# Kernel optimization log

Hardware: AMD Instinct MI355X
Metric: run time of the kernel (lower is better)

The kernel has to match this reference:

```python
import jax, jax.numpy as jnp
import numpy as np

# ---- module hyperparams (match init_kwargs) ----
IN_CH, OUT_CH = 32, 64
KERNEL = 9
STRIDE, PADDING = 1, 4
GRID_SIZE, SPLINE_ORDER = 5, 3
GRID_LO, GRID_HI = -1.0, 1.0
NUM_COEF = GRID_SIZE + SPLINE_ORDER  # 8 spline basis functions


def make_grid():
    h = (GRID_HI - GRID_LO) / GRID_SIZE
    # extended knot vector, same for every input feature (efficient-KAN)
    return (jnp.arange(-SPLINE_ORDER, GRID_SIZE + SPLINE_ORDER + 1, dtype=jnp.float32) * h + GRID_LO)


def b_splines(x, grid, order):
    """Cox-de Boor B-spline bases. x: (...,) -> (..., NUM_COEF)."""
    x = x[..., None]
    bases = ((x >= grid[:-1]) & (x < grid[1:])).astype(x.dtype)
    for k in range(1, order + 1):
        left = (x - grid[: -(k + 1)]) / (grid[k:-1] - grid[: -(k + 1)])
        right = (grid[k + 1:] - x) / (grid[k + 1:] - grid[1:-k])
        bases = left * bases[..., :-1] + right * bases[..., 1:]
    return bases


def setup_inputs() -> dict:
    key = jax.random.key(0)
    k1, k2, k3, k4 = jax.random.split(key, 4)
    x = jax.random.normal(k1, (16, IN_CH, 2048), dtype=jnp.float32)
    # all O*I KANLinear(kernel->1) modules batched into single tensors
    base_w = jax.random.normal(k2, (OUT_CH, IN_CH, KERNEL), dtype=jnp.float32) * (1.0 / np.sqrt(KERNEL))
    spline_w = jax.random.normal(k3, (OUT_CH, IN_CH, KERNEL, NUM_COEF), dtype=jnp.float32) * 0.1
    spline_scaler = jax.random.normal(k4, (OUT_CH, IN_CH, KERNEL), dtype=jnp.float32) * (1.0 / np.sqrt(KERNEL))
    return {"x": x, "base_w": base_w, "spline_w": spline_w, "spline_scaler": spline_scaler}


def reference(x, base_w, spline_w, spline_scaler):
    grid = make_grid()
    B, I, L = x.shape
    L_out = (L + 2 * PADDING - (KERNEL - 1) - 1) // STRIDE + 1  # dilation=1
    xp = jnp.pad(x, ((0, 0), (0, 0), (PADDING, PADDING)))
    # sliding windows: (B, I, L_out, K)
    idx = jnp.arange(L_out)[:, None] * STRIDE + jnp.arange(KERNEL)[None, :]
    win = xp[:, :, idx]
    # base branch: silu(window) . base_weight, summed over in_channels
    out = jnp.einsum('bilk,oik->bol', jax.nn.silu(win), base_w)
    # spline branch
    bs = b_splines(win, grid, SPLINE_ORDER)          # (B, I, L_out, K, C)
    sw = spline_w * spline_scaler[..., None]         # scaled spline weight
    out = out + jnp.einsum('bilkc,oikc->bol', bs, sw)
    return out
```

## Files before the change

### kernel.cpp

```cpp
#include <hip/hip_runtime.h>
#include <hip/hip_bf16.h>

namespace {

constexpr int KIN  = 32;
constexpr int KOUT = 64;
constexpr int KW   = 9;
constexpr int KPAD = 4;
constexpr int LIN  = 2048;
constexpr int KTOT = 2592;

typedef __bf16 bf16x8 __attribute__((ext_vector_type(8)));
typedef float  f32x4  __attribute__((ext_vector_type(4)));
typedef unsigned short u16x4 __attribute__((ext_vector_type(4)));
typedef unsigned short u16x8 __attribute__((ext_vector_type(8)));

__device__ __forceinline__ unsigned short f2bf(float x) {
    unsigned int u = __float_as_uint(x);
    u += 0x7FFFu + ((u >> 16) & 1u);
    return (unsigned short)(u >> 16);
}

__device__ __forceinline__ float bf2f(unsigned short h) {
    return __uint_as_float((unsigned int)h << 16);
}

#define MFMA16(a, b, c) __builtin_amdgcn_mfma_f32_16x16x32_bf16((a), (b), (c), 0, 0, 0)

__global__ __launch_bounds__(256) void kan_wprep(const float* __restrict__ base_w,
                                                 const float* __restrict__ spline_w,
                                                 const float* __restrict__ spline_scaler,
                                                 unsigned short* __restrict__ Wf) {
    unsigned int idx = blockIdx.x * 256 + threadIdx.x;
    unsigned int ch  = idx >> 8;
    unsigned int m   = (idx >> 6) & 3;
    unsigned int lane = idx & 63;
    unsigned int hi = lane >> 4, lo = lane & 15;
    unsigned int o  = m * 16 + lo;
    unsigned int kb = ch * 32 + hi * 8;

    u16x8 pk;
#pragma unroll
    for (int e = 0; e < 8; ++e) {
        unsigned int kappa = kb + e;
        unsigned int k  = kappa / 288;
        unsigned int r2 = kappa - k * 288;
        unsigned int i  = r2 / 9;
        unsigned int c  = r2 - i * 9;
        unsigned int t  = o * 288 + i * 9 + k;
        float val = (c == 0) ? base_w[t]
                             : spline_w[(size_t)t * 8 + (c - 1)] * spline_scaler[t];
        pk[e] = f2bf(val);
    }
    *(u16x8*)(Wf + (size_t)idx * 8) = pk;
}

constexpr int BN     = 64;
constexpr int TROW   = 72;
constexpr int F2COLS = 296;

__global__ __launch_bounds__(512, 4) void kan_fused(const float* __restrict__ x,
                                                    const unsigned short* __restrict__ Wf,
                                                    float* __restrict__ out) {
    __shared__ __align__(16) char smem[TROW * F2COLS * 2];
    unsigned short* f2t = (unsigned short*)smem;

    int tid  = threadIdx.x;
    int lane = tid & 63;
    int wv   = tid >> 6;
    int lo = lane & 15, hi = lane >> 4;

    int blk = blockIdx.x;
    int b   = blk >> 5;
    int l0  = (blk & 31) * BN;

    float vv[5];
#pragma unroll
    for (int p = 0; p < 5; ++p) {
        int unit = p * 512 + tid;
        bool ok = unit < TROW * KIN;
        int i = unit / TROW;
        int r = unit - i * TROW;
        int gx = l0 + r - KPAD;
        vv[p] = 0.f;
        if (ok && gx >= 0 && gx < LIN) vv[p] = x[((size_t)b * KIN + i) * LIN + gx];
    }

    {
        f32x4 z = (f32x4){0.f, 0.f, 0.f, 0.f};
        for (int c = tid; c < TROW * F2COLS / 8; c += 512)
            *(f32x4*)(f2t + (size_t)c * 8) = z;
    }
    __syncthreads();

#pragma unroll
    for (int p = 0; p < 5; ++p) {
        int unit = p * 512 + tid;
        bool ok = unit < TROW * KIN;
        int i = unit / TROW;
        int r = unit - i * TROW;
        float v = vv[p];
        if (ok) {
            unsigned short* row = f2t + (size_t)r * F2COLS + i * 9;
            row[0] = f2bf(v / (1.f + __expf(-v)));
            float t5 = (v + 2.2f) * 2.5f;
            float mf = floorf(t5);
            int   m  = (int)mf;
            float u  = t5 - mf;
            float u2 = u * u, u3 = u2 * u;
            float w  = 1.f - u;
            float P0 = u3 * (1.f / 6.f);
            float P3 = w * w * w * (1.f / 6.f);
            float P1 = (1.f / 6.f) + 0.5f * u + 0.5f * u2 - 0.5f * u3;
            float P2 = (4.f / 6.f) - u2 + 0.5f * u3;
            int c0 = m - 3;
            if ((unsigned)(c0 + 0) <= 7u) row[1 + c0 + 0] = f2bf(P3);
            if ((unsigned)(c0 + 1) <= 7u) row[1 + c0 + 1] = f2bf(P2);
            if ((unsigned)(c0 + 2) <= 7u) row[1 + c0 + 2] = f2bf(P1);
            if ((unsigned)(c0 + 3) <= 7u) row[1 + c0 + 3] = f2bf(P0);
        }
    }
    __syncthreads();

    const int ch0 = 10 * wv;
    constexpr int NCHW = 10;

    f32x4 acc[4][4];
#pragma unroll
    for (int m = 0; m < 4; ++m)
#pragma unroll
        for (int n = 0; n < 4; ++n) acc[m][n] = (f32x4){0.f, 0.f, 0.f, 0.f};

    int kk = ch0 / 9;
    int jb = ch0 - kk * 9;
    const unsigned short* wp = Wf + (size_t)ch0 * 2048 + (size_t)lane * 8;
    const unsigned short* fp = f2t + (size_t)(lo + kk) * F2COLS + jb * 32 + hi * 8;

    bf16x8 a0 = *(const bf16x8*)(wp);
    bf16x8 a1 = *(const bf16x8*)(wp + 512);
    bf16x8 a2 = *(const bf16x8*)(wp + 1024);
    bf16x8 a3 = *(const bf16x8*)(wp + 1536);
    bf16x8 b0 = *(const bf16x8*)(fp);
    bf16x8 b1 = *(const bf16x8*)(fp + 16 * F2COLS);
    bf16x8 b2 = *(const bf16x8*)(fp + 32 * F2COLS);
    bf16x8 b3 = *(const bf16x8*)(fp + 48 * F2COLS);

    for (int t = 0; t < NCHW; ++t) {
        bool last = (t + 1 == NCHW);
        const unsigned short* wpn = last ? wp : wp + 2048;
        int jb2 = last ? jb : jb + 1;
        const unsigned short* fpn = last ? fp : fp + ((jb2 == 9) ? (F2COLS - 8 * 32) : 32);
        if (jb2 == 9) jb2 = 0;

        bf16x8 na0 = *(const bf16x8*)(wpn);
        bf16x8 na1 = *(const bf16x8*)(wpn + 512);
        bf16x8 na2 = *(const bf16x8*)(wpn + 1024);
        bf16x8 na3 = *(const bf16x8*)(wpn + 1536);

        __builtin_amdgcn_s_setprio(1);
        acc[0][0] = MFMA16(a0, b0, acc[0][0]);
        acc[1][0] = MFMA16(a1, b0, acc[1][0]);
        acc[2][0] = MFMA16(a2, b0, acc[2][0]);
        acc[3][0] = MFMA16(a3, b0, acc[3][0]);
        b0 = *(const bf16x8*)(fpn);
        acc[0][1] = MFMA16(a0, b1, acc[0][1]);
        acc[1][1] = MFMA16(a1, b1, acc[1][1]);
        acc[2][1] = MFMA16(a2, b1, acc[2][1]);
        acc[3][1] = MFMA16(a3, b1, acc[3][1]);
        b1 = *(const bf16x8*)(fpn + 16 * F2COLS);
        acc[0][2] = MFMA16(a0, b2, acc[0][2]);
        acc[1][2] = MFMA16(a1, b2, acc[1][2]);
        acc[2][2] = MFMA16(a2, b2, acc[2][2]);
        acc[3][2] = MFMA16(a3, b2, acc[3][2]);
        b2 = *(const bf16x8*)(fpn + 32 * F2COLS);
        acc[0][3] = MFMA16(a0, b3, acc[0][3]);
        acc[1][3] = MFMA16(a1, b3, acc[1][3]);
        acc[2][3] = MFMA16(a2, b3, acc[2][3]);
        acc[3][3] = MFMA16(a3, b3, acc[3][3]);
        b3 = *(const bf16x8*)(fpn + 48 * F2COLS);
        __builtin_amdgcn_s_setprio(0);

        a0 = na0; a1 = na1; a2 = na2; a3 = na3;
        wp = wpn; fp = fpn; jb = jb2;
    }

    {
        int mq = wv & 3;
        int np = wv >> 2;
        bf16x8 a80 = *(const bf16x8*)(Wf + (size_t)80 * 2048 + (size_t)mq * 512 + (size_t)lane * 8);
        const unsigned short* fp80 = f2t + (size_t)(lo + 8) * F2COLS + 8 * 32 + hi * 8;
        bf16x8 bA = *(const bf16x8*)(fp80 + (size_t)(2 * np) * 16 * F2COLS);
        bf16x8 bB = *(const bf16x8*)(fp80 + (size_t)(2 * np + 1) * 16 * F2COLS);
        switch (wv) {
        case 0: acc[0][0] = MFMA16(a80, bA, acc[0][0]); acc[0][1] = MFMA16(a80, bB, acc[0][1]); break;
        case 1: acc[1][0] = MFMA16(a80, bA, acc[1][0]); acc[1][1] = MFMA16(a80, bB, acc[1][1]); break;
        case 2: acc[2][0] = MFMA16(a80, bA, acc[2][0]); acc[2][1] = MFMA16(a80, bB, acc[2][1]); break;
        case 3: acc[3][0] = MFMA16(a80, bA, acc[3][0]); acc[3][1] = MFMA16(a80, bB, acc[3][1]); break;
        case 4: acc[0][2] = MFMA16(a80, bA, acc[0][2]); acc[0][3] = MFMA16(a80, bB, acc[0][3]); break;
        case 5: acc[1][2] = MFMA16(a80, bA, acc[1][2]); acc[1][3] = MFMA16(a80, bB, acc[1][3]); break;
        case 6: acc[2][2] = MFMA16(a80, bA, acc[2][2]); acc[2][3] = MFMA16(a80, bB, acc[2][3]); break;
        case 7: acc[3][2] = MFMA16(a80, bA, acc[3][2]); acc[3][3] = MFMA16(a80, bB, acc[3][3]); break;
        }
    }

    __syncthreads();
    unsigned short* red16 = (unsigned short*)smem;
#pragma unroll
    for (int mp = 0; mp < 2; ++mp) {
#pragma unroll
        for (int dm = 0; dm < 2; ++dm)
#pragma unroll
            for (int n = 0; n < 4; ++n) {
                f32x4 a = acc[mp * 2 + dm][n];
                u16x4 pk = (u16x4){f2bf(a[0]), f2bf(a[1]), f2bf(a[2]), f2bf(a[3])};
                *(u16x4*)(red16 + (((size_t)wv * 8 + dm * 4 + n) * 64 + lane) * 4) = pk;
            }
        __syncthreads();
        {
            int dm = wv >> 2, n = wv & 3;
            f32x4 s = (f32x4){0.f, 0.f, 0.f, 0.f};
#pragma unroll
            for (int w = 0; w < 8; ++w) {
                u16x4 pk = *(const u16x4*)(red16 + (((size_t)w * 8 + dm * 4 + n) * 64 + lane) * 4);
                s[0] += bf2f(pk[0]);
                s[1] += bf2f(pk[1]);
                s[2] += bf2f(pk[2]);
                s[3] += bf2f(pk[3]);
            }
            int o = (mp * 2 + dm) * 16 + hi * 4;
            float* op = out + ((size_t)b * KOUT + o) * LIN + l0 + n * 16 + lo;
            op[0]               = s[0];
            op[LIN]             = s[1];
            op[2 * LIN]         = s[2];
            op[3 * (size_t)LIN] = s[3];
        }
        if (mp == 0) __syncthreads();
    }
}

}

extern "C" void kernel_launch(void* const* d_in, const int* in_sizes, int n_in,
                              void* d_out, int out_size, void* d_ws, size_t ws_size,
                              hipStream_t stream) {
    const float* x             = (const float*)d_in[0];
    const float* base_w        = (const float*)d_in[1];
    const float* spline_w      = (const float*)d_in[2];
    const float* spline_scaler = (const float*)d_in[3];
    float* out = (float*)d_out;

    unsigned short* Wf = (unsigned short*)d_ws;

    kan_wprep<<<81, 256, 0, stream>>>(base_w, spline_w, spline_scaler, Wf);
    kan_fused<<<512, 512, 0, stream>>>(x, Wf, out);
}
```

Before: 23.15 us.

## Fuse weight prep into main kernel with cross-block sentinel spin-wait

Removes the separate weight-prep launch: the first 81 blocks of the main kernel build the bf16 fused weight matrix and publish a per-block sentinel flag. All blocks build their B-spline tile first, then spin on the flags before the MFMA loop. This targets the launch gap and the serialization between the two kernels. The flags are never reset, so on later calls blocks may not wait for the current rewrite. The acquire side uses only relaxed loads, so memory ordering is weak.

```diff
diff --git a/kernel.cpp b/kernel.cpp
--- a/kernel.cpp
+++ b/kernel.cpp
@@ -9,6 +9,7 @@
 constexpr int KPAD = 4;
 constexpr int LIN  = 2048;
 constexpr int KTOT = 2592;
+constexpr unsigned MAGIC = 0x7F7F7F7Fu;
 
 typedef __bf16 bf16x8 __attribute__((ext_vector_type(8)));
 typedef float  f32x4  __attribute__((ext_vector_type(4)));
@@ -27,41 +28,17 @@
 
 #define MFMA16(a, b, c) __builtin_amdgcn_mfma_f32_16x16x32_bf16((a), (b), (c), 0, 0, 0)
 
-__global__ __launch_bounds__(256) void kan_wprep(const float* __restrict__ base_w,
-                                                 const float* __restrict__ spline_w,
-                                                 const float* __restrict__ spline_scaler,
-                                                 unsigned short* __restrict__ Wf) {
-    unsigned int idx = blockIdx.x * 256 + threadIdx.x;
-    unsigned int ch  = idx >> 8;
-    unsigned int m   = (idx >> 6) & 3;
-    unsigned int lane = idx & 63;
-    unsigned int hi = lane >> 4, lo = lane & 15;
-    unsigned int o  = m * 16 + lo;
-    unsigned int kb = ch * 32 + hi * 8;
-
-    u16x8 pk;
-#pragma unroll
-    for (int e = 0; e < 8; ++e) {
-        unsigned int kappa = kb + e;
-        unsigned int k  = kappa / 288;
-        unsigned int r2 = kappa - k * 288;
-        unsigned int i  = r2 / 9;
-        unsigned int c  = r2 - i * 9;
-        unsigned int t  = o * 288 + i * 9 + k;
-        float val = (c == 0) ? base_w[t]
-                             : spline_w[(size_t)t * 8 + (c - 1)] * spline_scaler[t];
-        pk[e] = f2bf(val);
-    }
-    *(u16x8*)(Wf + (size_t)idx * 8) = pk;
-}
-
 constexpr int BN     = 64;
 constexpr int TROW   = 72;
 constexpr int F2COLS = 296;
 
-__global__ __launch_bounds__(512, 4) void kan_fused(const float* __restrict__ x,
-                                                    const unsigned short* __restrict__ Wf,
-                                                    float* __restrict__ out) {
+__global__ __launch_bounds__(512, 4) void kan_all(const float* __restrict__ x,
+                                                  const float* __restrict__ base_w,
+                                                  const float* __restrict__ spline_w,
+                                                  const float* __restrict__ spline_scaler,
+                                                  unsigned short* __restrict__ Wf,
+                                                  unsigned int* __restrict__ sent,
+                                                  float* __restrict__ out) {
     __shared__ __align__(16) char smem[TROW * F2COLS * 2];
     unsigned short* f2t = (unsigned short*)smem;
 
@@ -73,6 +50,34 @@
     int blk = blockIdx.x;
     int b   = blk >> 5;
     int l0  = (blk & 31) * BN;
+
+    if (blk < 81) {
+        if (tid < 256) {
+            unsigned idx  = (unsigned)blk * 256 + tid;
+            unsigned m    = (idx >> 6) & 3;
+            unsigned ln   = idx & 63;
+            unsigned o    = m * 16 + (ln & 15);
+            unsigned kb   = (unsigned)blk * 32 + (ln >> 4) * 8;
+            u16x8 pk;
+#pragma unroll
+            for (int e = 0; e < 8; ++e) {
+                unsigned kappa = kb + e;
+                unsigned k  = kappa / 288;
+                unsigned r2 = kappa - k * 288;
+                unsigned i  = r2 / 9;
+                unsigned c  = r2 - i * 9;
+                unsigned t  = o * 288 + i * 9 + k;
+                float val = (c == 0) ? base_w[t]
+                                     : spline_w[(size_t)t * 8 + (c - 1)] * spline_scaler[t];
+                pk[e] = f2bf(val);
+            }
+            *(u16x8*)(Wf + (size_t)idx * 8) = pk;
+        }
+        __builtin_amdgcn_fence(__ATOMIC_RELEASE, "agent");
+        __syncthreads();
+        if (tid == 0)
+            __hip_atomic_store(&sent[blk], MAGIC, __ATOMIC_RELAXED, __HIP_MEMORY_SCOPE_AGENT);
+    }
 
     float vv[5];
 #pragma unroll
@@ -122,6 +127,13 @@
     }
     __syncthreads();
 
+    if (tid < 81) {
+        while (__hip_atomic_load(&sent[tid], __ATOMIC_RELAXED, __HIP_MEMORY_SCOPE_AGENT) != MAGIC)
+            __builtin_amdgcn_s_sleep(2);
+    }
+    __syncthreads();
+    asm volatile("" ::: "memory");
+
     const int ch0 = 10 * wv;
     constexpr int NCHW = 10;
 
@@ -249,8 +261,8 @@
     const float* spline_scaler = (const float*)d_in[3];
     float* out = (float*)d_out;
 
-    unsigned short* Wf = (unsigned short*)d_ws;
-
-    kan_wprep<<<81, 256, 0, stream>>>(base_w, spline_w, spline_scaler, Wf);
-    kan_fused<<<512, 512, 0, stream>>>(x, Wf, out);
-}
+    unsigned short* Wf  = (unsigned short*)d_ws;
+    unsigned int*  sent = (unsigned int*)((char*)d_ws + 331776);
+
+    kan_all<<<512, 512, 0, stream>>>(x, base_w, spline_w, spline_scaler, Wf, sent, out);
+}
```

New measurement: 32.52 us. 1.41x slower.

## Double output tile to 128 columns with 1024-thread blocks and hoisted weight loads

Applied to the files above, without the earlier changes.

Each block now covers 128 output positions with 16 waves: pairs of waves share a K-chunk and split the N dimension into two 64-column halves. This halves the grid to 256 blocks and amortizes the feature-tile halo over more columns. The initial weight-fragment loads are moved ahead of the feature construction so their global latency overlaps the LDS fill. The cross-wave reduction is restructured into two phases, one per half. The risk is a larger LDS footprint per block (about 80 KB) and fewer blocks than CUs, which may hurt occupancy and parallelism.

```diff
diff --git a/kernel.cpp b/kernel.cpp
--- a/kernel.cpp
+++ b/kernel.cpp
@@ -35,9 +35,8 @@
     unsigned int ch  = idx >> 8;
     unsigned int m   = (idx >> 6) & 3;
     unsigned int lane = idx & 63;
-    unsigned int hi = lane >> 4, lo = lane & 15;
-    unsigned int o  = m * 16 + lo;
-    unsigned int kb = ch * 32 + hi * 8;
+    unsigned int o  = m * 16 + (lane & 15);
+    unsigned int kb = ch * 32 + (lane >> 4) * 8;
 
     u16x8 pk;
 #pragma unroll
@@ -55,13 +54,13 @@
     *(u16x8*)(Wf + (size_t)idx * 8) = pk;
 }
 
-constexpr int BN     = 64;
-constexpr int TROW   = 72;
+constexpr int BN     = 128;
+constexpr int TROW   = 136;
 constexpr int F2COLS = 296;
 
-__global__ __launch_bounds__(512, 4) void kan_fused(const float* __restrict__ x,
-                                                    const unsigned short* __restrict__ Wf,
-                                                    float* __restrict__ out) {
+__global__ __launch_bounds__(1024, 4) void kan_fused(const float* __restrict__ x,
+                                                     const unsigned short* __restrict__ Wf,
+                                                     float* __restrict__ out) {
     __shared__ __align__(16) char smem[TROW * F2COLS * 2];
     unsigned short* f2t = (unsigned short*)smem;
 
@@ -69,15 +68,27 @@
     int lane = tid & 63;
     int wv   = tid >> 6;
     int lo = lane & 15, hi = lane >> 4;
+    int kg = wv >> 1;
+    int nh = wv & 1;
 
     int blk = blockIdx.x;
-    int b   = blk >> 5;
-    int l0  = (blk & 31) * BN;
+    int b   = blk >> 4;
+    int l0  = (blk & 15) * BN;
+
+    const int ch0 = 10 * kg;
+    constexpr int NCHW = 10;
+    int kk = ch0 / 9;
+    int jb = ch0 - kk * 9;
+    const unsigned short* wp = Wf + (size_t)ch0 * 2048 + (size_t)lane * 8;
+    bf16x8 a0 = *(const bf16x8*)(wp);
+    bf16x8 a1 = *(const bf16x8*)(wp + 512);
+    bf16x8 a2 = *(const bf16x8*)(wp + 1024);
+    bf16x8 a3 = *(const bf16x8*)(wp + 1536);
 
     float vv[5];
 #pragma unroll
     for (int p = 0; p < 5; ++p) {
-        int unit = p * 512 + tid;
+        int unit = p * 1024 + tid;
         bool ok = unit < TROW * KIN;
         int i = unit / TROW;
         int r = unit - i * TROW;
@@ -88,14 +99,14 @@
 
     {
         f32x4 z = (f32x4){0.f, 0.f, 0.f, 0.f};
-        for (int c = tid; c < TROW * F2COLS / 8; c += 512)
+        for (int c = tid; c < TROW * F2COLS / 8; c += 1024)
             *(f32x4*)(f2t + (size_t)c * 8) = z;
     }
     __syncthreads();
 
 #pragma unroll
     for (int p = 0; p < 5; ++p) {
-        int unit = p * 512 + tid;
+        int unit = p * 1024 + tid;
         bool ok = unit < TROW * KIN;
         int i = unit / TROW;
         int r = unit - i * TROW;
@@ -122,24 +133,13 @@
     }
     __syncthreads();
 
-    const int ch0 = 10 * wv;
-    constexpr int NCHW = 10;
-
     f32x4 acc[4][4];
 #pragma unroll
     for (int m = 0; m < 4; ++m)
 #pragma unroll
         for (int n = 0; n < 4; ++n) acc[m][n] = (f32x4){0.f, 0.f, 0.f, 0.f};
 
-    int kk = ch0 / 9;
-    int jb = ch0 - kk * 9;
-    const unsigned short* wp = Wf + (size_t)ch0 * 2048 + (size_t)lane * 8;
-    const unsigned short* fp = f2t + (size_t)(lo + kk) * F2COLS + jb * 32 + hi * 8;
-
-    bf16x8 a0 = *(const bf16x8*)(wp);
-    bf16x8 a1 = *(const bf16x8*)(wp + 512);
-    bf16x8 a2 = *(const bf16x8*)(wp + 1024);
-    bf16x8 a3 = *(const bf16x8*)(wp + 1536);
+    const unsigned short* fp = f2t + (size_t)(nh * 64 + lo + kk) * F2COLS + jb * 32 + hi * 8;
     bf16x8 b0 = *(const bf16x8*)(fp);
     bf16x8 b1 = *(const bf16x8*)(fp + 16 * F2COLS);
     bf16x8 b2 = *(const bf16x8*)(fp + 32 * F2COLS);
@@ -185,13 +185,13 @@
     }
 
     {
-        int mq = wv & 3;
-        int np = wv >> 2;
+        int mq = kg & 3;
+        int np = kg >> 2;
         bf16x8 a80 = *(const bf16x8*)(Wf + (size_t)80 * 2048 + (size_t)mq * 512 + (size_t)lane * 8);
-        const unsigned short* fp80 = f2t + (size_t)(lo + 8) * F2COLS + 8 * 32 + hi * 8;
+        const unsigned short* fp80 = f2t + (size_t)(nh * 64 + lo + 8) * F2COLS + 8 * 32 + hi * 8;
         bf16x8 bA = *(const bf16x8*)(fp80 + (size_t)(2 * np) * 16 * F2COLS);
         bf16x8 bB = *(const bf16x8*)(fp80 + (size_t)(2 * np + 1) * 16 * F2COLS);
-        switch (wv) {
+        switch (kg) {
         case 0: acc[0][0] = MFMA16(a80, bA, acc[0][0]); acc[0][1] = MFMA16(a80, bB, acc[0][1]); break;
         case 1: acc[1][0] = MFMA16(a80, bA, acc[1][0]); acc[1][1] = MFMA16(a80, bB, acc[1][1]); break;
         case 2: acc[2][0] = MFMA16(a80, bA, acc[2][0]); acc[2][1] = MFMA16(a80, bB, acc[2][1]); break;
@@ -206,35 +206,39 @@
     __syncthreads();
     unsigned short* red16 = (unsigned short*)smem;
 #pragma unroll
-    for (int mp = 0; mp < 2; ++mp) {
-#pragma unroll
-        for (int dm = 0; dm < 2; ++dm)
-#pragma unroll
-            for (int n = 0; n < 4; ++n) {
-                f32x4 a = acc[mp * 2 + dm][n];
-                u16x4 pk = (u16x4){f2bf(a[0]), f2bf(a[1]), f2bf(a[2]), f2bf(a[3])};
-                *(u16x4*)(red16 + (((size_t)wv * 8 + dm * 4 + n) * 64 + lane) * 4) = pk;
-            }
+    for (int ph = 0; ph < 2; ++ph) {
+        if (nh == ph) {
+#pragma unroll
+            for (int m = 0; m < 4; ++m)
+#pragma unroll
+                for (int n = 0; n < 4; ++n) {
+                    int sid = m * 4 + n;
+                    f32x4 a = acc[m][n];
+                    u16x4 pk = (u16x4){f2bf(a[0]), f2bf(a[1]), f2bf(a[2]), f2bf(a[3])};
+                    *(u16x4*)(red16 + (((size_t)sid * 8 + kg) * 64 + lane) * 4) = pk;
+                }
+        }
         __syncthreads();
         {
-            int dm = wv >> 2, n = wv & 3;
+            int sid = wv;
+            int m = sid >> 2, n = sid & 3;
             f32x4 s = (f32x4){0.f, 0.f, 0.f, 0.f};
 #pragma unroll
             for (int w = 0; w < 8; ++w) {
-                u16x4 pk = *(const u16x4*)(red16 + (((size_t)w * 8 + dm * 4 + n) * 64 + lane) * 4);
+                u16x4 pk = *(const u16x4*)(red16 + (((size_t)sid * 8 + w) * 64 + lane) * 4);
                 s[0] += bf2f(pk[0]);
                 s[1] += bf2f(pk[1]);
                 s[2] += bf2f(pk[2]);
                 s[3] += bf2f(pk[3]);
             }
-            int o = (mp * 2 + dm) * 16 + hi * 4;
-            float* op = out + ((size_t)b * KOUT + o) * LIN + l0 + n * 16 + lo;
+            int o = m * 16 + hi * 4;
+            float* op = out + ((size_t)b * KOUT + o) * LIN + l0 + ph * 64 + n * 16 + lo;
             op[0]               = s[0];
             op[LIN]             = s[1];
             op[2 * LIN]         = s[2];
             op[3 * (size_t)LIN] = s[3];
         }
-        if (mp == 0) __syncthreads();
+        if (ph == 0) __syncthreads();
     }
 }
 
@@ -252,5 +256,5 @@
     unsigned short* Wf = (unsigned short*)d_ws;
 
     kan_wprep<<<81, 256, 0, stream>>>(base_w, spline_w, spline_scaler, Wf);
-    kan_fused<<<512, 512, 0, stream>>>(x, Wf, out);
-}
+    kan_fused<<<256, 1024, 0, stream>>>(x, Wf, out);
+}
```

Result: slower. 24.67 us (+6.6%).

## Switch GEMM core to 32x32x16 bf16 MFMA tiles

Applied to the files above, without the earlier changes.

Replaces the 16x16x32 MFMA tiling with 32x32x16 bf16 MFMA, so each wave holds four 32x32 accumulators instead of sixteen 16x16 ones. The weight prep layout, the LDS feature indexing, the tail chunk handling and the cross-wave reduction are all rewritten to match the new fragment layout. Weight A-fragment loads are also issued earlier, before the spline-basis construction, to hide global latency. The intent is fewer MFMA issues and fewer operand loads per FLOP. The cost is longer per-instruction latency over a short 20-step loop, plus new reduction indexing.

```diff
diff --git a/kernel.cpp b/kernel.cpp
--- a/kernel.cpp
+++ b/kernel.cpp
@@ -12,6 +12,7 @@
 
 typedef __bf16 bf16x8 __attribute__((ext_vector_type(8)));
 typedef float  f32x4  __attribute__((ext_vector_type(4)));
+typedef float  f32x16 __attribute__((ext_vector_type(16)));
 typedef unsigned short u16x4 __attribute__((ext_vector_type(4)));
 typedef unsigned short u16x8 __attribute__((ext_vector_type(8)));
 
@@ -25,19 +26,18 @@
     return __uint_as_float((unsigned int)h << 16);
 }
 
-#define MFMA16(a, b, c) __builtin_amdgcn_mfma_f32_16x16x32_bf16((a), (b), (c), 0, 0, 0)
+#define MFMA32(a, b, c) __builtin_amdgcn_mfma_f32_32x32x16_bf16((a), (b), (c), 0, 0, 0)
 
 __global__ __launch_bounds__(256) void kan_wprep(const float* __restrict__ base_w,
                                                  const float* __restrict__ spline_w,
                                                  const float* __restrict__ spline_scaler,
                                                  unsigned short* __restrict__ Wf) {
     unsigned int idx = blockIdx.x * 256 + threadIdx.x;
-    unsigned int ch  = idx >> 8;
-    unsigned int m   = (idx >> 6) & 3;
-    unsigned int lane = idx & 63;
-    unsigned int hi = lane >> 4, lo = lane & 15;
-    unsigned int o  = m * 16 + lo;
-    unsigned int kb = ch * 32 + hi * 8;
+    unsigned int ch  = idx >> 7;
+    unsigned int mb  = (idx >> 6) & 1;
+    unsigned int l   = idx & 63;
+    unsigned int o   = mb * 32 + (l & 31);
+    unsigned int kb  = ch * 16 + (l >> 5) * 8;
 
     u16x8 pk;
 #pragma unroll
@@ -68,11 +68,20 @@
     int tid  = threadIdx.x;
     int lane = tid & 63;
     int wv   = tid >> 6;
-    int lo = lane & 15, hi = lane >> 4;
+    int l31  = lane & 31;
+    int hi2  = lane >> 5;
 
     int blk = blockIdx.x;
     int b   = blk >> 5;
     int l0  = (blk & 31) * BN;
+
+    const int ch0 = 20 * wv;
+    constexpr int NCHW = 20;
+    int kk = ch0 / 18;
+    int jb = ch0 - kk * 18;
+    const unsigned short* wp = Wf + (size_t)ch0 * 1024 + (size_t)lane * 8;
+    bf16x8 a0 = *(const bf16x8*)(wp);
+    bf16x8 a1 = *(const bf16x8*)(wp + 512);
 
     float vv[5];
 #pragma unroll
@@ -122,84 +131,51 @@
     }
     __syncthreads();
 
-    const int ch0 = 10 * wv;
-    constexpr int NCHW = 10;
-
-    f32x4 acc[4][4];
-#pragma unroll
-    for (int m = 0; m < 4; ++m)
-#pragma unroll
-        for (int n = 0; n < 4; ++n) acc[m][n] = (f32x4){0.f, 0.f, 0.f, 0.f};
-
-    int kk = ch0 / 9;
-    int jb = ch0 - kk * 9;
-    const unsigned short* wp = Wf + (size_t)ch0 * 2048 + (size_t)lane * 8;
-    const unsigned short* fp = f2t + (size_t)(lo + kk) * F2COLS + jb * 32 + hi * 8;
-
-    bf16x8 a0 = *(const bf16x8*)(wp);
-    bf16x8 a1 = *(const bf16x8*)(wp + 512);
-    bf16x8 a2 = *(const bf16x8*)(wp + 1024);
-    bf16x8 a3 = *(const bf16x8*)(wp + 1536);
+    f32x16 acc00 = {}, acc01 = {}, acc10 = {}, acc11 = {};
+
+    const unsigned short* fp = f2t + (size_t)(l31 + kk) * F2COLS + jb * 16 + hi2 * 8;
     bf16x8 b0 = *(const bf16x8*)(fp);
-    bf16x8 b1 = *(const bf16x8*)(fp + 16 * F2COLS);
-    bf16x8 b2 = *(const bf16x8*)(fp + 32 * F2COLS);
-    bf16x8 b3 = *(const bf16x8*)(fp + 48 * F2COLS);
+    bf16x8 b1 = *(const bf16x8*)(fp + 32 * F2COLS);
 
     for (int t = 0; t < NCHW; ++t) {
         bool last = (t + 1 == NCHW);
-        const unsigned short* wpn = last ? wp : wp + 2048;
+        const unsigned short* wpn = last ? wp : wp + 1024;
         int jb2 = last ? jb : jb + 1;
-        const unsigned short* fpn = last ? fp : fp + ((jb2 == 9) ? (F2COLS - 8 * 32) : 32);
-        if (jb2 == 9) jb2 = 0;
+        const unsigned short* fpn = last ? fp : fp + ((jb2 == 18) ? 24 : 16);
+        if (jb2 == 18) jb2 = 0;
 
         bf16x8 na0 = *(const bf16x8*)(wpn);
         bf16x8 na1 = *(const bf16x8*)(wpn + 512);
-        bf16x8 na2 = *(const bf16x8*)(wpn + 1024);
-        bf16x8 na3 = *(const bf16x8*)(wpn + 1536);
 
         __builtin_amdgcn_s_setprio(1);
-        acc[0][0] = MFMA16(a0, b0, acc[0][0]);
-        acc[1][0] = MFMA16(a1, b0, acc[1][0]);
-        acc[2][0] = MFMA16(a2, b0, acc[2][0]);
-        acc[3][0] = MFMA16(a3, b0, acc[3][0]);
+        acc00 = MFMA32(a0, b0, acc00);
+        acc10 = MFMA32(a1, b0, acc10);
         b0 = *(const bf16x8*)(fpn);
-        acc[0][1] = MFMA16(a0, b1, acc[0][1]);
-        acc[1][1] = MFMA16(a1, b1, acc[1][1]);
-        acc[2][1] = MFMA16(a2, b1, acc[2][1]);
-        acc[3][1] = MFMA16(a3, b1, acc[3][1]);
-        b1 = *(const bf16x8*)(fpn + 16 * F2COLS);
-        acc[0][2] = MFMA16(a0, b2, acc[0][2]);
-        acc[1][2] = MFMA16(a1, b2, acc[1][2]);
-        acc[2][2] = MFMA16(a2, b2, acc[2][2]);
-        acc[3][2] = MFMA16(a3, b2, acc[3][2]);
-        b2 = *(const bf16x8*)(fpn + 32 * F2COLS);
-        acc[0][3] = MFMA16(a0, b3, acc[0][3]);
-        acc[1][3] = MFMA16(a1, b3, acc[1][3]);
-        acc[2][3] = MFMA16(a2, b3, acc[2][3]);
-        acc[3][3] = MFMA16(a3, b3, acc[3][3]);
-        b3 = *(const bf16x8*)(fpn + 48 * F2COLS);
+        acc01 = MFMA32(a0, b1, acc01);
+        acc11 = MFMA32(a1, b1, acc11);
+        b1 = *(const bf16x8*)(fpn + 32 * F2COLS);
         __builtin_amdgcn_s_setprio(0);
 
-        a0 = na0; a1 = na1; a2 = na2; a3 = na3;
+        a0 = na0; a1 = na1;
         wp = wpn; fp = fpn; jb = jb2;
     }
 
     {
-        int mq = wv & 3;
-        int np = wv >> 2;
-        bf16x8 a80 = *(const bf16x8*)(Wf + (size_t)80 * 2048 + (size_t)mq * 512 + (size_t)lane * 8);
-        const unsigned short* fp80 = f2t + (size_t)(lo + 8) * F2COLS + 8 * 32 + hi * 8;
-        bf16x8 bA = *(const bf16x8*)(fp80 + (size_t)(2 * np) * 16 * F2COLS);
-        bf16x8 bB = *(const bf16x8*)(fp80 + (size_t)(2 * np + 1) * 16 * F2COLS);
+        int chT = 160 + (wv >> 2);
+        int jbT = 16 + (wv >> 2);
+        int mbT = (wv >> 1) & 1;
+        int nbT = wv & 1;
+        bf16x8 aT = *(const bf16x8*)(Wf + ((size_t)chT * 2 + mbT) * 512 + (size_t)lane * 8);
+        bf16x8 bT = *(const bf16x8*)(f2t + (size_t)(nbT * 32 + l31 + 8) * F2COLS + jbT * 16 + hi2 * 8);
         switch (wv) {
-        case 0: acc[0][0] = MFMA16(a80, bA, acc[0][0]); acc[0][1] = MFMA16(a80, bB, acc[0][1]); break;
-        case 1: acc[1][0] = MFMA16(a80, bA, acc[1][0]); acc[1][1] = MFMA16(a80, bB, acc[1][1]); break;
-        case 2: acc[2][0] = MFMA16(a80, bA, acc[2][0]); acc[2][1] = MFMA16(a80, bB, acc[2][1]); break;
-        case 3: acc[3][0] = MFMA16(a80, bA, acc[3][0]); acc[3][1] = MFMA16(a80, bB, acc[3][1]); break;
-        case 4: acc[0][2] = MFMA16(a80, bA, acc[0][2]); acc[0][3] = MFMA16(a80, bB, acc[0][3]); break;
-        case 5: acc[1][2] = MFMA16(a80, bA, acc[1][2]); acc[1][3] = MFMA16(a80, bB, acc[1][3]); break;
-        case 6: acc[2][2] = MFMA16(a80, bA, acc[2][2]); acc[2][3] = MFMA16(a80, bB, acc[2][3]); break;
-        case 7: acc[3][2] = MFMA16(a80, bA, acc[3][2]); acc[3][3] = MFMA16(a80, bB, acc[3][3]); break;
+        case 0: acc00 = MFMA32(aT, bT, acc00); break;
+        case 1: acc01 = MFMA32(aT, bT, acc01); break;
+        case 2: acc10 = MFMA32(aT, bT, acc10); break;
+        case 3: acc11 = MFMA32(aT, bT, acc11); break;
+        case 4: acc00 = MFMA32(aT, bT, acc00); break;
+        case 5: acc01 = MFMA32(aT, bT, acc01); break;
+        case 6: acc10 = MFMA32(aT, bT, acc10); break;
+        case 7: acc11 = MFMA32(aT, bT, acc11); break;
         }
     }
 
@@ -207,28 +183,36 @@
     unsigned short* red16 = (unsigned short*)smem;
 #pragma unroll
     for (int mp = 0; mp < 2; ++mp) {
-#pragma unroll
-        for (int dm = 0; dm < 2; ++dm)
-#pragma unroll
-            for (int n = 0; n < 4; ++n) {
-                f32x4 a = acc[mp * 2 + dm][n];
-                u16x4 pk = (u16x4){f2bf(a[0]), f2bf(a[1]), f2bf(a[2]), f2bf(a[3])};
-                *(u16x4*)(red16 + (((size_t)wv * 8 + dm * 4 + n) * 64 + lane) * 4) = pk;
+        f32x16 wA = (mp == 0) ? acc00 : acc10;
+        f32x16 wB = (mp == 0) ? acc01 : acc11;
+        {
+            unsigned short* s0 = red16 + (((size_t)(0 * 8 + wv)) * 64 + lane) * 16;
+            unsigned short* s1 = red16 + (((size_t)(1 * 8 + wv)) * 64 + lane) * 16;
+#pragma unroll
+            for (int g = 0; g < 4; ++g) {
+                u16x4 pA = (u16x4){f2bf(wA[g * 4 + 0]), f2bf(wA[g * 4 + 1]),
+                                   f2bf(wA[g * 4 + 2]), f2bf(wA[g * 4 + 3])};
+                u16x4 pB = (u16x4){f2bf(wB[g * 4 + 0]), f2bf(wB[g * 4 + 1]),
+                                   f2bf(wB[g * 4 + 2]), f2bf(wB[g * 4 + 3])};
+                *(u16x4*)(s0 + g * 4) = pA;
+                *(u16x4*)(s1 + g * 4) = pB;
             }
+        }
         __syncthreads();
         {
-            int dm = wv >> 2, n = wv & 3;
+            int nb = wv & 1;
+            int q  = wv >> 1;
             f32x4 s = (f32x4){0.f, 0.f, 0.f, 0.f};
 #pragma unroll
             for (int w = 0; w < 8; ++w) {
-                u16x4 pk = *(const u16x4*)(red16 + (((size_t)w * 8 + dm * 4 + n) * 64 + lane) * 4);
+                u16x4 pk = *(const u16x4*)(red16 + (((size_t)(nb * 8 + w)) * 64 + lane) * 16 + q * 4);
                 s[0] += bf2f(pk[0]);
                 s[1] += bf2f(pk[1]);
                 s[2] += bf2f(pk[2]);
                 s[3] += bf2f(pk[3]);
             }
-            int o = (mp * 2 + dm) * 16 + hi * 4;
-            float* op = out + ((size_t)b * KOUT + o) * LIN + l0 + n * 16 + lo;
+            int o = mp * 32 + 8 * q + 4 * hi2;
+            float* op = out + ((size_t)b * KOUT + o) * LIN + l0 + nb * 32 + l31;
             op[0]               = s[0];
             op[LIN]             = s[1];
             op[2 * LIN]         = s[2];
```

Result: slower. 25.71 us (+11.1%).
